# Optimization experiments

Measured on AMD Instinct MI355X. Metric: run time of the kernel, lower is better.

Reference implementation:

```python
import jax, jax.numpy as jnp
import numpy as np

T, B, A = 256, 2048, 18
GAMMA = 0.99   # discount_factor
COEF = 0.01    # entropy coefficient


def setup_inputs() -> dict:
    key = jax.random.key(0)
    ks = jax.random.split(key, 7)
    policy = jax.nn.softmax(jax.random.normal(ks[0], (T, B, A), jnp.float32), axis=-1)
    behavior_policy = jax.nn.softmax(jax.random.normal(ks[1], (T, B, A), jnp.float32), axis=-1)
    rewards = jax.random.normal(ks[2], (T, B), jnp.float32)
    values = jax.random.normal(ks[3], (T, B), jnp.float32)
    next_values = jax.random.normal(ks[4], (T, B), jnp.float32)
    actions = jax.random.randint(ks[5], (T, B), 0, A)
    done = jax.random.bernoulli(ks[6], 0.02, (T, B))
    return dict(policy=policy, behavior_policy=behavior_policy, rewards=rewards,
                values=values, next_values=next_values, actions=actions, done=done)


def _gather(p, a):
    # p: [T,B,A], a: [T,B] -> [T,B] probability of taken action
    return jnp.take_along_axis(p, a[..., None], axis=-1)[..., 0]


def reference(policy, behavior_policy, rewards, values, next_values, actions, done):
    dt = values.dtype
    clipped_rewards = jnp.clip(rewards, -1.0, 1.0)          # reward_clip='abs_one'
    discounts = (~done).astype(dt) * GAMMA                  # [T,B]

    # ---- V-trace (computed under no_grad in the original) ----
    log_rhos = jnp.log(_gather(policy, actions)) - jnp.log(_gather(behavior_policy, actions))
    rhos = jnp.exp(log_rhos)
    clipped_rhos = jnp.minimum(1.0, rhos)                   # clip_rho_threshold = 1.0
    cs = jnp.minimum(1.0, rhos)
    values_t1 = jnp.concatenate([values[1:], next_values[-1:]], axis=0)
    deltas = clipped_rhos * (clipped_rewards + discounts * values_t1 - values)

    def step(acc, x):
        d, disc, c = x
        v = d + disc * c * acc   # acc = vs_minus_v_xs[t+1]; acc=0 at t=T-1 -> deltas[-1]
        return v, v

    _, vs_mv = jax.lax.scan(step, jnp.zeros_like(values[0]), (deltas, discounts, cs), reverse=True)
    vs = jax.lax.stop_gradient(vs_mv + values)
    pg_adv_vt = jax.lax.stop_gradient(clipped_rhos * (clipped_rewards + discounts * next_values - values))

    # ---- train() combines the v-trace outputs into the loss ----
    pg_advantage = pg_adv_vt * (clipped_rewards + GAMMA * (1.0 - done.astype(dt)) * vs - values)
    value_loss = jnp.mean((vs - values) ** 2)
    entropy_loss = -jnp.mean(jnp.sum(policy * jnp.log(policy + 1e-10), axis=-1))
    policy_loss = -jnp.mean(pg_advantage * jnp.log(_gather(policy, actions)))
    return policy_loss + value_loss + COEF * entropy_loss
```

## Files before the change

### kernel.cpp

```cpp
#include <hip/hip_runtime.h>
#include <stdint.h>

#define TT 256
#define BB 2048
#define AA 18
#define NTB (TT * BB)
#define WPB 4
#define SEGLEN 2
#define TPB 8
#define NTBLK 32
#define NBLK 1024
#define LN2 0.69314718055994531f


__global__ __launch_bounds__(256) void main_k(
    const float* __restrict__ policy,
    const float* __restrict__ behavior,
    const float* __restrict__ rewards,
    const float* __restrict__ values,
    const float* __restrict__ next_values,
    const int* __restrict__ actions,
    const void* __restrict__ done,
    float* __restrict__ pe, float* __restrict__ pv, float* __restrict__ pp,
    float* __restrict__ wsf)
{
    int tid = threadIdx.x;
    int lane = tid & 63;
    int w = tid >> 6;
    int bid = blockIdx.x;
    int g = bid >> 5;
    int tb = bid & 31;

    __shared__ float tup[WPB][5][64];
    __shared__ float red[WPB][3];

    const int* di = (const int*)done;
    int bad = 0;
#pragma unroll
    for (int i = 0; i < 16; ++i) {
        int v = di[lane + 64 * i];
        bad |= !(v == 0 || v == 1 || v == 0x3F800000);
    }
    bool bytelay = (__any(bad) != 0);
    const uint8_t* d8 = (const uint8_t*)done;

    int b = g * 64 + lane;
    int tA = tb * TPB + w * SEGLEN + 1;
    int tB = tA - 1;
    int rA = tA * BB + b, rB = tB * BB + b;

    int aA = actions[rA], aB = actions[rB];
    float piA = policy[(size_t)rA * AA + aA];
    float muA = behavior[(size_t)rA * AA + aA];
    float piB = policy[(size_t)rB * AA + aB];
    float muB = behavior[(size_t)rB * AA + aB];
    float rwA = rewards[rA], rwB = rewards[rB];
    float v0A = values[rA],  v0B = values[rB];
    float nvA = next_values[rA], nvB = next_values[rB];
    int dnA = bytelay ? (int)d8[rA] : di[rA];
    int dnB = bytelay ? (int)d8[rB] : di[rB];
    float vtA = (tA == TT - 1) ? nvA : values[rA + BB];
    float vtB = v0A;

    float ent2 = 0.f, vacc = 0.f, P = 1.f;
    float sv0 = 0.f, sv1 = 0.f, sv2 = 0.f, sp0 = 0.f, sp1 = 0.f;

    auto entropy_tile = [&](int t) {
        const float* gsrc = policy + (size_t)(t * BB + g * 64) * AA;
#pragma unroll
        for (int k = 0; k < 9; ++k) {
            float2 v = *(const float2*)(gsrc + 2 * (lane + 64 * k));
            ent2 = fmaf(v.x, __log2f(v.x + 1e-10f), ent2);
            ent2 = fmaf(v.y, __log2f(v.y + 1e-10f), ent2);
        }
    };

    auto step = [&](float pi, float mu, float rw, float v0, float nv,
                    int dn, float vt1) {
        float lpi = LN2 * __log2f(pi + 1e-10f);
        float c = fminf(1.0f, pi / mu);
        float disc = dn ? 0.f : 0.99f;
        float cr = fminf(1.f, fmaxf(-1.f, rw));
        float base = cr - v0;
        float dlt = c * fmaf(disc, vt1, base);
        float gg = disc * c;
        vacc = fmaf(gg, vacc, dlt);
        P *= gg;
        sv0 = fmaf(vacc, vacc, sv0);
        sv1 = fmaf(P, vacc, sv1);
        sv2 = fmaf(P, P, sv2);
        float adv = c * fmaf(disc, nv, base);
        float q = fmaf(disc, v0, base);
        float al = adv * lpi;
        sp0 = fmaf(al, fmaf(disc, vacc, q), sp0);
        sp1 = fmaf(al * disc, P, sp1);
    };

    entropy_tile(tA);
    entropy_tile(tB);
    step(piA, muA, rwA, v0A, nvA, dnA, vtA);
    step(piB, muB, rwB, v0B, nvB, dnB, vtB);

    tup[w][0][lane] = P;
    tup[w][1][lane] = vacc;
    tup[w][2][lane] = sv1;
    tup[w][3][lane] = sv2;
    tup[w][4][lane] = sp1;
    float ent = LN2 * ent2;
    for (int off = 32; off > 0; off >>= 1) {
        ent += __shfl_down(ent, off);
        sv0 += __shfl_down(sv0, off);
        sp0 += __shfl_down(sp0, off);
    }
    if (lane == 0) { red[w][0] = ent; red[w][1] = sv0; red[w][2] = sp0; }
    __syncthreads();

    if (w == 0) {
        float A  = tup[3][0][lane];
        float Bv = tup[3][1][lane];
        float s1 = tup[3][2][lane];
        float s2 = tup[3][3][lane];
        float p1 = tup[3][4][lane];
        float svx = 0.f, spx = 0.f;
#pragma unroll
        for (int s = WPB - 2; s >= 0; --s) {
            float Al  = tup[s][0][lane];
            float Bl  = tup[s][1][lane];
            float s1l = tup[s][2][lane];
            float s2l = tup[s][3][lane];
            float p1l = tup[s][4][lane];
            svx = fmaf(2.f * Bv, s1l, svx);
            svx = fmaf(Bv * Bv, s2l, svx);
            spx = fmaf(Bv, p1l, spx);
            s1 = fmaf(A, fmaf(Bv, s2l, s1l), s1);
            s2 = fmaf(A * A, s2l, s2);
            p1 = fmaf(A, p1l, p1);
            Bv = fmaf(Al, Bv, Bl);
            A  = A * Al;
        }
        int col = g * 64 + lane;
        wsf[(0 * NTBLK + tb) * BB + col] = A;
        wsf[(1 * NTBLK + tb) * BB + col] = Bv;
        wsf[(2 * NTBLK + tb) * BB + col] = s1;
        wsf[(3 * NTBLK + tb) * BB + col] = s2;
        wsf[(4 * NTBLK + tb) * BB + col] = p1;
        for (int off = 32; off > 0; off >>= 1) {
            svx += __shfl_down(svx, off);
            spx += __shfl_down(spx, off);
        }
        if (lane == 0) {
            pe[bid] = red[0][0] + red[1][0] + red[2][0] + red[3][0];
            pv[bid] = red[0][1] + red[1][1] + red[2][1] + red[3][1] + svx;
            pp[bid] = red[0][2] + red[1][2] + red[2][2] + red[3][2] + spx;
        }
    }
}

__global__ __launch_bounds__(256) void fold_k(
    const float* __restrict__ wsf,
    float* __restrict__ fsv, float* __restrict__ fsp)
{
    int tid = threadIdx.x;
    int col = blockIdx.x * 256 + tid;
    float C = 0.f, svT = 0.f, spT = 0.f;
#pragma unroll 8
    for (int tb2 = NTBLK - 1; tb2 >= 0; --tb2) {
        float A  = wsf[(0 * NTBLK + tb2) * BB + col];
        float Bv = wsf[(1 * NTBLK + tb2) * BB + col];
        float s1 = wsf[(2 * NTBLK + tb2) * BB + col];
        float s2 = wsf[(3 * NTBLK + tb2) * BB + col];
        float p1 = wsf[(4 * NTBLK + tb2) * BB + col];
        svT = fmaf(2.f * C, s1, svT);
        svT = fmaf(C * C, s2, svT);
        spT = fmaf(C, p1, spT);
        C = fmaf(A, C, Bv);
    }
    for (int off = 32; off > 0; off >>= 1) {
        svT += __shfl_down(svT, off);
        spT += __shfl_down(spT, off);
    }
    __shared__ float s1r[4], s2r[4];
    int lane = tid & 63, w = tid >> 6;
    if (lane == 0) { s1r[w] = svT; s2r[w] = spT; }
    __syncthreads();
    if (tid == 0) {
        fsv[blockIdx.x] = s1r[0] + s1r[1] + s1r[2] + s1r[3];
        fsp[blockIdx.x] = s2r[0] + s2r[1] + s2r[2] + s2r[3];
    }
}

__global__ __launch_bounds__(256) void final_k(
    const float* __restrict__ pe, const float* __restrict__ pv,
    const float* __restrict__ pp, const float* __restrict__ fsv,
    const float* __restrict__ fsp, float* __restrict__ out)
{
    int tid = threadIdx.x;
    float e = 0.f, v = 0.f, p = 0.f;
#pragma unroll
    for (int i = 0; i < NBLK / 256; ++i) {
        int j = tid + 256 * i;
        e += pe[j];
        v += pv[j];
        p += pp[j];
    }
    if (tid < 8) { v += fsv[tid]; p += fsp[tid]; }
    for (int off = 32; off > 0; off >>= 1) {
        e += __shfl_down(e, off);
        v += __shfl_down(v, off);
        p += __shfl_down(p, off);
    }
    __shared__ float s0[4], s1[4], s2[4];
    int lane = tid & 63, w = tid >> 6;
    if (lane == 0) { s0[w] = e; s1[w] = v; s2[w] = p; }
    __syncthreads();
    if (tid == 0) {
        double E  = (double)s0[0] + s0[1] + s0[2] + s0[3];
        double V  = (double)s1[0] + s1[1] + s1[2] + s1[3];
        double Pp = (double)s2[0] + s2[1] + s2[2] + s2[3];
        out[0] = (float)((V - Pp - 0.01 * E) / (double)NTB);
    }
}

extern "C" void kernel_launch(void* const* d_in, const int* in_sizes, int n_in,
                              void* d_out, int out_size, void* d_ws, size_t ws_size,
                              hipStream_t stream) {
    const float* policy      = (const float*)d_in[0];
    const float* behavior    = (const float*)d_in[1];
    const float* rewards     = (const float*)d_in[2];
    const float* values      = (const float*)d_in[3];
    const float* next_values = (const float*)d_in[4];
    const int*   actions     = (const int*)d_in[5];
    const void*  done        = d_in[6];

    float* pe  = (float*)d_ws;
    float* pv  = pe + NBLK;
    float* pp  = pv + NBLK;
    float* fsv = pp + NBLK;
    float* fsp = fsv + 8;
    float* wsf = fsp + 8;

    main_k<<<NBLK, 256, 0, stream>>>(policy, behavior, rewards, values,
                                     next_values, actions, done,
                                     pe, pv, pp, wsf);
    fold_k<<<8, 256, 0, stream>>>(wsf, fsv, fsp);
    final_k<<<1, 256, 0, stream>>>(pe, pv, pp, fsv, fsp, (float*)d_out);
}
```

Before: 28.49 us.

## Use 1024-thread blocks covering 32 timesteps and merge fold and final kernels

Each main-kernel block now has 16 waves covering 32 timesteps, so there are 256 blocks instead of 1024 and the number of time-block partials per column drops from 32 to 8. The separate fold and final-reduction kernels are merged into one single-block 1024-thread kernel, which removes one launch and the intermediate workspace round trip. The trade-offs are a longer serial combine in wave 0 (15 steps), fewer blocks to spread across CUs, and a single-block tail doing both the column fold and the final reduction.

```diff
diff --git a/kernel.cpp b/kernel.cpp
--- a/kernel.cpp
+++ b/kernel.cpp
@@ -5,15 +5,15 @@
 #define BB 2048
 #define AA 18
 #define NTB (TT * BB)
-#define WPB 4
+#define WPB 16
 #define SEGLEN 2
-#define TPB 8
-#define NTBLK 32
-#define NBLK 1024
+#define TPB 32
+#define NTBLK 8
+#define NBLK 256
 #define LN2 0.69314718055994531f
 
 
-__global__ __launch_bounds__(256) void main_k(
+__global__ __launch_bounds__(1024) void main_k(
     const float* __restrict__ policy,
     const float* __restrict__ behavior,
     const float* __restrict__ rewards,
@@ -28,8 +28,8 @@
     int lane = tid & 63;
     int w = tid >> 6;
     int bid = blockIdx.x;
-    int g = bid >> 5;
-    int tb = bid & 31;
+    int g = bid >> 3;
+    int tb = bid & 7;
 
     __shared__ float tup[WPB][5][64];
     __shared__ float red[WPB][3];
@@ -116,11 +116,11 @@
     __syncthreads();
 
     if (w == 0) {
-        float A  = tup[3][0][lane];
-        float Bv = tup[3][1][lane];
-        float s1 = tup[3][2][lane];
-        float s2 = tup[3][3][lane];
-        float p1 = tup[3][4][lane];
+        float A  = tup[15][0][lane];
+        float Bv = tup[15][1][lane];
+        float s1 = tup[15][2][lane];
+        float s2 = tup[15][3][lane];
+        float p1 = tup[15][4][lane];
         float svx = 0.f, spx = 0.f;
 #pragma unroll
         for (int s = WPB - 2; s >= 0; --s) {
@@ -144,79 +144,67 @@
         wsf[(2 * NTBLK + tb) * BB + col] = s1;
         wsf[(3 * NTBLK + tb) * BB + col] = s2;
         wsf[(4 * NTBLK + tb) * BB + col] = p1;
+
         for (int off = 32; off > 0; off >>= 1) {
             svx += __shfl_down(svx, off);
             spx += __shfl_down(spx, off);
         }
+        float eT = 0.f, vT = 0.f, pT = 0.f;
+        if (lane < WPB) { eT = red[lane][0]; vT = red[lane][1]; pT = red[lane][2]; }
+        for (int off = 8; off > 0; off >>= 1) {
+            eT += __shfl_down(eT, off);
+            vT += __shfl_down(vT, off);
+            pT += __shfl_down(pT, off);
+        }
         if (lane == 0) {
-            pe[bid] = red[0][0] + red[1][0] + red[2][0] + red[3][0];
-            pv[bid] = red[0][1] + red[1][1] + red[2][1] + red[3][1] + svx;
-            pp[bid] = red[0][2] + red[1][2] + red[2][2] + red[3][2] + spx;
+            pe[bid] = eT;
+            pv[bid] = vT + svx;
+            pp[bid] = pT + spx;
         }
     }
 }
 
-__global__ __launch_bounds__(256) void fold_k(
+__global__ __launch_bounds__(1024) void fold2_k(
     const float* __restrict__ wsf,
-    float* __restrict__ fsv, float* __restrict__ fsp)
+    const float* __restrict__ pe, const float* __restrict__ pv,
+    const float* __restrict__ pp, float* __restrict__ out)
 {
     int tid = threadIdx.x;
-    int col = blockIdx.x * 256 + tid;
-    float C = 0.f, svT = 0.f, spT = 0.f;
-#pragma unroll 8
-    for (int tb2 = NTBLK - 1; tb2 >= 0; --tb2) {
-        float A  = wsf[(0 * NTBLK + tb2) * BB + col];
-        float Bv = wsf[(1 * NTBLK + tb2) * BB + col];
-        float s1 = wsf[(2 * NTBLK + tb2) * BB + col];
-        float s2 = wsf[(3 * NTBLK + tb2) * BB + col];
-        float p1 = wsf[(4 * NTBLK + tb2) * BB + col];
-        svT = fmaf(2.f * C, s1, svT);
-        svT = fmaf(C * C, s2, svT);
-        spT = fmaf(C, p1, spT);
-        C = fmaf(A, C, Bv);
-    }
-    for (int off = 32; off > 0; off >>= 1) {
-        svT += __shfl_down(svT, off);
-        spT += __shfl_down(spT, off);
-    }
-    __shared__ float s1r[4], s2r[4];
-    int lane = tid & 63, w = tid >> 6;
-    if (lane == 0) { s1r[w] = svT; s2r[w] = spT; }
-    __syncthreads();
-    if (tid == 0) {
-        fsv[blockIdx.x] = s1r[0] + s1r[1] + s1r[2] + s1r[3];
-        fsp[blockIdx.x] = s2r[0] + s2r[1] + s2r[2] + s2r[3];
-    }
-}
-
-__global__ __launch_bounds__(256) void final_k(
-    const float* __restrict__ pe, const float* __restrict__ pv,
-    const float* __restrict__ pp, const float* __restrict__ fsv,
-    const float* __restrict__ fsp, float* __restrict__ out)
-{
-    int tid = threadIdx.x;
-    float e = 0.f, v = 0.f, p = 0.f;
-#pragma unroll
-    for (int i = 0; i < NBLK / 256; ++i) {
-        int j = tid + 256 * i;
-        e += pe[j];
-        v += pv[j];
-        p += pp[j];
-    }
-    if (tid < 8) { v += fsv[tid]; p += fsp[tid]; }
+    float svT = 0.f, spT = 0.f;
+#pragma unroll
+    for (int cc = 0; cc < 2; ++cc) {
+        int col = tid + cc * 1024;
+        float C = 0.f;
+#pragma unroll
+        for (int tb2 = NTBLK - 1; tb2 >= 0; --tb2) {
+            float A  = wsf[(0 * NTBLK + tb2) * BB + col];
+            float Bv = wsf[(1 * NTBLK + tb2) * BB + col];
+            float s1 = wsf[(2 * NTBLK + tb2) * BB + col];
+            float s2 = wsf[(3 * NTBLK + tb2) * BB + col];
+            float p1 = wsf[(4 * NTBLK + tb2) * BB + col];
+            svT = fmaf(2.f * C, s1, svT);
+            svT = fmaf(C * C, s2, svT);
+            spT = fmaf(C, p1, spT);
+            C = fmaf(A, C, Bv);
+        }
+    }
+    float e = 0.f, v = svT, p = spT;
+    if (tid < NBLK) { e = pe[tid]; v += pv[tid]; p += pp[tid]; }
     for (int off = 32; off > 0; off >>= 1) {
         e += __shfl_down(e, off);
         v += __shfl_down(v, off);
         p += __shfl_down(p, off);
     }
-    __shared__ float s0[4], s1[4], s2[4];
+    __shared__ float red2[16][3];
     int lane = tid & 63, w = tid >> 6;
-    if (lane == 0) { s0[w] = e; s1[w] = v; s2[w] = p; }
+    if (lane == 0) { red2[w][0] = e; red2[w][1] = v; red2[w][2] = p; }
     __syncthreads();
     if (tid == 0) {
-        double E  = (double)s0[0] + s0[1] + s0[2] + s0[3];
-        double V  = (double)s1[0] + s1[1] + s1[2] + s1[3];
-        double Pp = (double)s2[0] + s2[1] + s2[2] + s2[3];
+        double E = 0.0, V = 0.0, Pp = 0.0;
+#pragma unroll
+        for (int i = 0; i < 16; ++i) {
+            E += red2[i][0]; V += red2[i][1]; Pp += red2[i][2];
+        }
         out[0] = (float)((V - Pp - 0.01 * E) / (double)NTB);
     }
 }
@@ -235,13 +223,10 @@
     float* pe  = (float*)d_ws;
     float* pv  = pe + NBLK;
     float* pp  = pv + NBLK;
-    float* fsv = pp + NBLK;
-    float* fsp = fsv + 8;
-    float* wsf = fsp + 8;
-
-    main_k<<<NBLK, 256, 0, stream>>>(policy, behavior, rewards, values,
-                                     next_values, actions, done,
-                                     pe, pv, pp, wsf);
-    fold_k<<<8, 256, 0, stream>>>(wsf, fsv, fsp);
-    final_k<<<1, 256, 0, stream>>>(pe, pv, pp, fsv, fsp, (float*)d_out);
+    float* wsf = pp + NBLK;
+
+    main_k<<<NBLK, 1024, 0, stream>>>(policy, behavior, rewards, values,
+                                      next_values, actions, done,
+                                      pe, pv, pp, wsf);
+    fold2_k<<<1, 1024, 0, stream>>>(wsf, pe, pv, pp, (float*)d_out);
 }
```

After: 28.09 us. About the same (-1.4%).
